# Performance work log

Hardware: AMD Instinct MI355X
Metric: run time of the kernel (lower is better)

## Reference

```python
import jax, jax.numpy as jnp
import numpy as np

N_SERIES = 1024  # N; x carries 3N stacked time-synchronous nodes
GCN_DEPTH = 2
IN_DIM = 64
H_DIM = 64


def setup_inputs() -> dict:
    key = jax.random.key(0)
    k = jax.random.split(key, 6)
    B, C, N3 = 64, IN_DIM, 3 * N_SERIES
    x = jax.random.normal(k[0], (N3, B, C), dtype=jnp.float32)
    A = jax.random.normal(k[1], (N3, N3), dtype=jnp.float32) * 0.02
    # Linear2d (1x1 conv) params per depth; act='glu' -> out = 2*h_dim
    s0 = 1.0 / np.sqrt(IN_DIM)
    s1 = 1.0 / np.sqrt(H_DIM)
    W0 = jax.random.uniform(k[2], (2 * H_DIM, IN_DIM), jnp.float32, -s0, s0)
    b0 = jax.random.uniform(k[3], (2 * H_DIM,), jnp.float32, -s0, s0)
    W1 = jax.random.uniform(k[4], (2 * H_DIM, H_DIM), jnp.float32, -s1, s1)
    b1 = jax.random.uniform(k[5], (2 * H_DIM,), jnp.float32, -s1, s1)
    return {"x": x, "A": A, "W0": W0, "b0": b0, "W1": W1, "b1": b1}


def reference(x, A, W0, b0, W1, b1):
    # x: (3N, B, C) -> (B, C, 3N)
    h = jnp.transpose(x, (1, 2, 0))
    convs = []
    for W, b in ((W0, b0), (W1, b1)):
        # GCN2d flow='tgt_to_src': h[b,c,v] = sum_w h[b,c,w] * A[v,w]  (L=1 squeezed)
        g = jnp.einsum('bcw,vw->bcv', h, A)
        # Linear2d 1x1 conv: channels C -> 2*h_dim, then GLU gate
        y = jnp.einsum('oc,bcv->bov', W, g) + b[None, :, None]
        lhs, rhs = jnp.split(y, 2, axis=1)
        h = lhs * jax.nn.sigmoid(rhs)          # (B, h_dim, 3N)
        convs.append(jnp.transpose(h, (2, 0, 1)))  # (3N, B, h_dim)
    # crop the middle N nodes of each depth, then max over depth
    cropped = jnp.stack([c[N_SERIES:2 * N_SERIES] for c in convs], axis=0)
    return jnp.max(cropped, axis=0)  # (N, B, h_dim)
```

## Files before the change

### kernel.cpp

```cpp
#include <hip/hip_runtime.h>
#include <hip/hip_bf16.h>
#include <stdint.h>

typedef __attribute__((ext_vector_type(8))) short s16x8;
typedef __attribute__((ext_vector_type(4))) float f32x4;
typedef __attribute__((ext_vector_type(8))) unsigned short u16x8;
typedef __attribute__((ext_vector_type(4))) unsigned short u16x4;

__device__ __forceinline__ float bf2f(unsigned short u) {
  union { uint32_t u; float f; } v; v.u = ((uint32_t)u) << 16; return v.f;
}
__device__ __forceinline__ unsigned short f2bf(float f) {
  union { float f; uint32_t u; } v; v.f = f;
  uint32_t u = v.u;
  return (unsigned short)((u + 0x7fffu + ((u >> 16) & 1u)) >> 16);
}
__device__ __forceinline__ void load_lds16(const void* g, void* l) {
  __builtin_amdgcn_global_load_lds(
      (const __attribute__((address_space(1))) void*)g,
      (__attribute__((address_space(3))) void*)l, 16, 0, 0);
}

template <int N>
__device__ __forceinline__ void vmw() {
  if constexpr (N == 0) asm volatile("s_waitcnt vmcnt(0)" ::: "memory");
  else if constexpr (N == 1) asm volatile("s_waitcnt vmcnt(1)" ::: "memory");
  else if constexpr (N == 2) asm volatile("s_waitcnt vmcnt(2)" ::: "memory");
  else if constexpr (N == 3) asm volatile("s_waitcnt vmcnt(3)" ::: "memory");
  else if constexpr (N == 4) asm volatile("s_waitcnt vmcnt(4)" ::: "memory");
  else if constexpr (N == 5) asm volatile("s_waitcnt vmcnt(5)" ::: "memory");
  else if constexpr (N == 6) asm volatile("s_waitcnt vmcnt(6)" ::: "memory");
  else if constexpr (N == 7) asm volatile("s_waitcnt vmcnt(7)" ::: "memory");
  else asm volatile("s_waitcnt vmcnt(8)" ::: "memory");
}
#define SBAR() asm volatile("s_barrier" ::: "memory")


__global__ void k_detect(const uint32_t* __restrict__ xw, int* __restrict__ flag) {
  int lane = threadIdx.x;
  uint32_t u = xw[lane * 97 + 1];
  int e = (u >> 7) & 0xFF;
  unsigned long long m = __ballot(e > 150);
  if (lane == 0) *flag = (__popcll(m) > 6) ? 1 : 0;
}

__global__ __launch_bounds__(256) void k_prep(const void* __restrict__ xin,
                                              const void* __restrict__ Ain,
                                              const void* __restrict__ W0,
                                              const void* __restrict__ b0,
                                              const void* __restrict__ W1,
                                              const void* __restrict__ b1,
                                              unsigned short* __restrict__ xtp,
                                              unsigned short* __restrict__ Abp,
                                              unsigned short* __restrict__ wb,
                                              const int* __restrict__ flag) {
  __shared__ __align__(16) unsigned short sh[64 * 65];
  const int t = threadIdx.x;
  const int bid = blockIdx.x;
  const int fp = *flag;

  if (bid < 3072) {
    const int w0 = (bid % 48) * 64;
    const int m0 = (bid / 48) * 64;
    if (fp) {
      const float* xf = (const float*)xin;
#pragma unroll
      for (int rep = 0; rep < 4; ++rep) {
        int vi = t + rep * 256;
        int r = vi >> 4;
        int c4 = (vi & 15) * 4;
        f32x4 v = *(const f32x4*)(xf + (uint64_t)(w0 + r) * 4096 + m0 + c4);
#pragma unroll
        for (int u = 0; u < 4; ++u) sh[(c4 + u) * 65 + r] = f2bf(v[u]);
      }
    } else {
      const unsigned short* xb = (const unsigned short*)xin;
#pragma unroll
      for (int rep = 0; rep < 2; ++rep) {
        int vi = t + rep * 256;
        int r = vi >> 3;
        int c8 = (vi & 7) * 8;
        u16x8 v = *(const u16x8*)(xb + (uint64_t)(w0 + r) * 4096 + m0 + c8);
#pragma unroll
        for (int u = 0; u < 8; ++u) sh[(c8 + u) * 65 + r] = v[u];
      }
    }
    __syncthreads();
    unsigned short* dst = xtp + ((uint64_t)(m0 >> 6) * 48 + (w0 >> 6)) * 4096;
#pragma unroll
    for (int rep = 0; rep < 2; ++rep) {
      int vi = t + rep * 256;
      int kb = vi >> 6, r = vi & 63;
      u16x8 v;
#pragma unroll
      for (int u = 0; u < 8; ++u) v[u] = sh[r * 65 + kb * 8 + u];
      *(u16x8*)(dst + kb * 512 + r * 8) = v;
    }
  } else if (bid < 5376) {
    const int b2 = bid - 3072;
    const int kt = b2 % 48, rt = b2 / 48;
    if (fp) {
      const float* Af = (const float*)Ain;
#pragma unroll
      for (int rep = 0; rep < 4; ++rep) {
        int vi = t + rep * 256;
        int r = vi >> 4;
        int c4 = (vi & 15) * 4;
        f32x4 v = *(const f32x4*)(Af + (uint64_t)(rt * 64 + r) * 3072 + kt * 64 + c4);
        int kb = c4 >> 3, e = c4 & 7;
#pragma unroll
        for (int u = 0; u < 4; ++u) sh[kb * 520 + r * 8 + e + u] = f2bf(v[u]);
      }
    } else {
      const unsigned short* Ab16 = (const unsigned short*)Ain;
#pragma unroll
      for (int rep = 0; rep < 2; ++rep) {
        int vi = t + rep * 256;
        int r = vi >> 3;
        int c8 = (vi & 7) * 8;
        u16x8 v = *(const u16x8*)(Ab16 + (uint64_t)(rt * 64 + r) * 3072 + kt * 64 + c8);
#pragma unroll
        for (int u = 0; u < 8; ++u) sh[(c8 >> 3) * 520 + r * 8 + u] = v[u];
      }
    }
    __syncthreads();
    unsigned short* dst = Abp + ((uint64_t)rt * 48 + kt) * 4096;
#pragma unroll
    for (int rep = 0; rep < 2; ++rep) {
      int vi = t + rep * 256;
      int kb = vi >> 6, r = vi & 63;
      u16x8 v;
#pragma unroll
      for (int u = 0; u < 8; ++u) v[u] = sh[kb * 520 + r * 8 + u];
      *(u16x8*)(dst + kb * 512 + r * 8) = v;
    }
  } else {
    for (int i = t; i < 16640; i += 256) {
      const void* src; int off;
      if (i < 8192)        { src = W0; off = i; }
      else if (i < 8320)   { src = b0; off = i - 8192; }
      else if (i < 16512)  { src = W1; off = i - 8320; }
      else                 { src = b1; off = i - 16512; }
      wb[i] = fp ? f2bf(((const float*)src)[off]) : ((const unsigned short*)src)[off];
    }
  }
}

template <int BM, int KTOT>
__global__ __launch_bounds__(512, 2) void k_gemm_glu2(
    const unsigned short* __restrict__ Am,
    const unsigned short* __restrict__ Bm,
    const unsigned short* __restrict__ W,
    const unsigned short* __restrict__ bias,
    unsigned short* __restrict__ H,
    int Vtot) {
  constexpr int BN  = 256;
  constexpr int IF  = BM / 32;
  constexpr int NPH = (IF > 4) ? 2 : 1;
  constexpr int IPH = IF / NPH;
  constexpr int APL = (BM / 64) * 4;
  constexpr int P   = APL + 16;
  constexpr int QF  = P / 8;
  constexpr int QR  = P - QF * 8;
  constexpr int PPW = QF + (QR ? 1 : 0);
  constexpr int BUFS = P * 512;
  constexpr int NT  = KTOT / 32;
  constexpr int Kt  = KTOT / 64;
  constexpr int NRB = BM / 16;
  constexpr int EPL = BM * 264;
  constexpr int SME = (4 * BUFS > EPL) ? 4 * BUFS : EPL;

  __shared__ __align__(16) unsigned short smem[SME];

  const int t    = threadIdx.x;
  const int lane = t & 63;
  const int wid  = t >> 6;
  const int wV   = wid >> 2;
  const int wM   = wid & 3;
  const int fr   = lane & 15;
  const int q4   = lane >> 4;
  const int v0   = blockIdx.x * BM;
  const int m0   = blockIdx.y * BN;
  const int art0 = v0 >> 6;
  const int brt0 = m0 >> 6;

  const int myq = QF + ((QR && wid < QR) ? 1 : 0);
  const unsigned short* srcb[PPW];
  int ldso[PPW];
#pragma unroll
  for (int q = 0; q < PPW; ++q) {
    int pi = wid + 8 * q;
    if (pi >= P) pi = P - 1;
    const int isA = pi < APL;
    const int rtl = (isA ? pi : pi - APL) >> 2;
    const int pb  = pi & 3;
    const unsigned short* base =
        isA ? (Am + (uint64_t)(art0 + rtl) * Kt * 4096)
            : (Bm + (uint64_t)(brt0 + rtl) * Kt * 4096);
    srcb[q] = base + pb * 512 + lane * 8;
    ldso[q] = pi * 512;
  }

  int aoff[IF], boff[4];
#pragma unroll
  for (int i = 0; i < IF; ++i) {
    const int row = wV * (BM / 2) + i * 16 + fr;
    aoff[i] = ((row >> 6) * 4 + q4) * 512 + (row & 63) * 8;
  }
#pragma unroll
  for (int j = 0; j < 4; ++j)
    boff[j] = (APL + wM * 4 + q4) * 512 + (j * 16 + fr) * 8;

  f32x4 acc[IF][4] = {};

#pragma unroll
  for (int pt = 0; pt < 3; ++pt)
#pragma unroll
    for (int q = 0; q < PPW; ++q)
      if (q < myq)
        load_lds16(srcb[q] + pt * 2048, smem + pt * BUFS + ldso[q]);
  if (QR && wid < QR) { vmw<2 * (QF + 1)>(); } else { vmw<2 * QF>(); }
  SBAR();

#pragma unroll 4
  for (int tt = 0; tt < NT; ++tt) {
    const unsigned short* buf = smem + (tt & 3) * BUFS;
    s16x8 bfr[4];
#pragma unroll
    for (int ph = 0; ph < NPH; ++ph) {
      if (ph == 0) {
#pragma unroll
        for (int j = 0; j < 4; ++j)
          bfr[j] = *(const s16x8*)(buf + boff[j]);
      }
      s16x8 afr[IPH];
#pragma unroll
      for (int ii = 0; ii < IPH; ++ii)
        afr[ii] = *(const s16x8*)(buf + aoff[ph * IPH + ii]);
      if (tt + 3 < NT) {
        unsigned short* dst = smem + ((tt + 3) & 3) * BUFS;
#pragma unroll
        for (int q = 0; q < PPW; ++q)
          if ((q % NPH) == ph && q < myq)
            load_lds16(srcb[q] + (uint64_t)(tt + 3) * 2048, dst + ldso[q]);
      }
      SBAR();
      __builtin_amdgcn_s_setprio(1);
#pragma unroll
      for (int ii = 0; ii < IPH; ++ii)
#pragma unroll
        for (int j = 0; j < 4; ++j)
          acc[ph * IPH + ii][j] = __builtin_amdgcn_mfma_f32_16x16x32_bf16(
              afr[ii], bfr[j], acc[ph * IPH + ii][j], 0, 0, 0);
      __builtin_amdgcn_s_setprio(0);
      if (ph == NPH - 1) {
        if (tt + 3 < NT) {
          if (QR && wid < QR) { vmw<2 * (QF + 1)>(); } else { vmw<2 * QF>(); }
        } else if (tt + 2 < NT) {
          if (QR && wid < QR) { vmw<QF + 1>(); } else { vmw<QF>(); }
        } else {
          vmw<0>();
        }
      }
      SBAR();
    }
  }

  {
    const int rr = q4 * 4;
#pragma unroll
    for (int i = 0; i < IF; ++i)
#pragma unroll
      for (int j = 0; j < 4; ++j) {
        const int col = wM * 64 + j * 16 + fr;
#pragma unroll
        for (int r = 0; r < 4; ++r) {
          const int row = wV * (BM / 2) + i * 16 + rr + r;
          smem[row * 264 + col] = f2bf(acc[i][j][r]);
        }
      }
  }
  __syncthreads();

  s16x8 wf[2][8];
#pragma unroll
  for (int ksi = 0; ksi < 2; ++ksi)
#pragma unroll
    for (int j = 0; j < 8; ++j)
      wf[ksi][j] = *(const s16x8*)(W + (j * 16 + fr) * 64 + ksi * 32 + q4 * 8);
  float bj[8];
#pragma unroll
  for (int j = 0; j < 8; ++j) bj[j] = bf2f(bias[j * 16 + fr]);

  const int Vt = Vtot >> 6;
#pragma unroll
  for (int rep = 0; rep < (NRB + 7) / 8; ++rep) {
    const int rb = rep * 8 + wid;
    if (rb < NRB) {
#pragma unroll
      for (int bb = 0; bb < 4; ++bb) {
        f32x4 acc2[8] = {};
#pragma unroll
        for (int ksi = 0; ksi < 2; ++ksi) {
          s16x8 af = *(const s16x8*)(smem + (rb * 16 + fr) * 264 + bb * 64 +
                                     ksi * 32 + q4 * 8);
#pragma unroll
          for (int j = 0; j < 8; ++j)
            acc2[j] = __builtin_amdgcn_mfma_f32_16x16x32_bf16(af, wf[ksi][j],
                                                              acc2[j], 0, 0, 0);
        }
        const int v = v0 + rb * 16 + q4 * 4;
#pragma unroll
        for (int j = 0; j < 4; ++j) {
          u16x4 pk;
#pragma unroll
          for (int r = 0; r < 4; ++r) {
            float lhs = acc2[j][r] + bj[j];
            float rhs = acc2[j + 4][r] + bj[j + 4];
            float sg = 1.0f / (1.0f + __expf(-rhs));
            pk[r] = f2bf(lhs * sg);
          }
          const int o = j * 16 + fr;
          const int hrow = m0 + bb * 64 + o;
          *(u16x4*)(H + ((uint64_t)(hrow >> 6) * Vt + (v >> 6)) * 4096 +
                    ((v >> 3) & 7) * 512 + (hrow & 63) * 8 + (v & 7)) = pk;
        }
      }
    }
  }
}

__global__ __launch_bounds__(256) void k_maxout(const unsigned short* __restrict__ H1,
                                                const unsigned short* __restrict__ H2,
                                                float* __restrict__ out) {
  __shared__ __align__(16) float tile[64 * 65];
  const int t = threadIdx.x;
  const int b = blockIdx.y;
  const int n0 = blockIdx.x * 64;
  {
    int j = t >> 2, p = t & 3;
    int c1 = 1024 + n0 + p * 16;
    int c2 = n0 + p * 16;
    const unsigned short* h1p =
        H1 + ((uint64_t)b * 48 + (c1 >> 6)) * 4096 + ((c1 >> 3) & 7) * 512 + j * 8;
    const unsigned short* h2p =
        H2 + ((uint64_t)b * 16 + (c2 >> 6)) * 4096 + ((c2 >> 3) & 7) * 512 + j * 8;
    u16x8 a0 = *(const u16x8*)(h1p);
    u16x8 a1 = *(const u16x8*)(h1p + 512);
    u16x8 c0 = *(const u16x8*)(h2p);
    u16x8 c1v = *(const u16x8*)(h2p + 512);
#pragma unroll
    for (int u = 0; u < 8; ++u) {
      tile[j * 65 + p * 16 + u] = fmaxf(bf2f(a0[u]), bf2f(c0[u]));
      tile[j * 65 + p * 16 + 8 + u] = fmaxf(bf2f(a1[u]), bf2f(c1v[u]));
    }
  }
  __syncthreads();
  {
    int n = t >> 2, jb = (t & 3) * 16;
    float* op = out + (uint64_t)(n0 + n) * 4096 + b * 64 + jb;
#pragma unroll
    for (int q = 0; q < 4; ++q) {
      f32x4 o;
#pragma unroll
      for (int u = 0; u < 4; ++u) o[u] = tile[(jb + q * 4 + u) * 65 + n];
      *(f32x4*)(op + q * 4) = o;
    }
  }
}

extern "C" void kernel_launch(void* const* d_in, const int* in_sizes, int n_in,
                              void* d_out, int out_size, void* d_ws, size_t ws_size,
                              hipStream_t stream) {
  (void)in_sizes; (void)n_in; (void)out_size; (void)ws_size;
  const void* x  = d_in[0];
  const void* A  = d_in[1];
  const void* W0 = d_in[2];
  const void* b0 = d_in[3];
  const void* W1 = d_in[4];
  const void* b1 = d_in[5];
  float* out = (float*)d_out;

  char* ws = (char*)d_ws;
  unsigned short* Xtp = (unsigned short*)(ws + 0);
  unsigned short* H2p = (unsigned short*)(ws + 0);
  unsigned short* Abp = (unsigned short*)(ws + 25165824);
  unsigned short* Wb  = (unsigned short*)(ws + 44040192);
  unsigned short* H1p = (unsigned short*)(ws + 44105728);
  int* flag = (int*)(ws + 69271552);

  k_detect<<<1, 64, 0, stream>>>((const uint32_t*)x, flag);
  k_prep<<<5377, 256, 0, stream>>>(x, A, W0, b0, W1, b1, Xtp, Abp, Wb, flag);
  k_gemm_glu2<192, 3072><<<dim3(16, 16), 512, 0, stream>>>(
      Abp, Xtp, Wb, Wb + 8192, H1p, 3072);
  k_gemm_glu2<64, 3072><<<dim3(16, 16), 512, 0, stream>>>(
      Abp + (uint64_t)16 * 48 * 4096, H1p, Wb + 8320, Wb + 16512, H2p, 1024);
  k_maxout<<<dim3(16, 64), 256, 0, stream>>>(H1p, H2p, out);
}
```

Before: 274.8 us.

## Software-pipeline LDS fragment loads in GEMM and fold dtype detection into prep

Measured after the change: 280.1 us. Within noise of the previous version (+2.0%).

```diff
diff --git a/kernel.cpp b/kernel.cpp
--- a/kernel.cpp
+++ b/kernel.cpp
@@ -36,14 +36,6 @@
 #define SBAR() asm volatile("s_barrier" ::: "memory")
 
 
-__global__ void k_detect(const uint32_t* __restrict__ xw, int* __restrict__ flag) {
-  int lane = threadIdx.x;
-  uint32_t u = xw[lane * 97 + 1];
-  int e = (u >> 7) & 0xFF;
-  unsigned long long m = __ballot(e > 150);
-  if (lane == 0) *flag = (__popcll(m) > 6) ? 1 : 0;
-}
-
 __global__ __launch_bounds__(256) void k_prep(const void* __restrict__ xin,
                                               const void* __restrict__ Ain,
                                               const void* __restrict__ W0,
@@ -52,12 +44,17 @@
                                               const void* __restrict__ b1,
                                               unsigned short* __restrict__ xtp,
                                               unsigned short* __restrict__ Abp,
-                                              unsigned short* __restrict__ wb,
-                                              const int* __restrict__ flag) {
+                                              unsigned short* __restrict__ wb) {
   __shared__ __align__(16) unsigned short sh[64 * 65];
   const int t = threadIdx.x;
   const int bid = blockIdx.x;
-  const int fp = *flag;
+  int fp;
+  {
+    uint32_t u = ((const uint32_t*)xin)[(t & 63) * 97 + 1];
+    int e = (u >> 7) & 0xFF;
+    unsigned long long m = __ballot(e > 150);
+    fp = (__popcll(m) > 6) ? 1 : 0;
+  }
 
   if (bid < 3072) {
     const int w0 = (bid % 48) * 64;
@@ -147,7 +144,7 @@
 }
 
 template <int BM, int KTOT>
-__global__ __launch_bounds__(512, 2) void k_gemm_glu2(
+__global__ __launch_bounds__(512, 2) void k_gemm_glu3(
     const unsigned short* __restrict__ Am,
     const unsigned short* __restrict__ Bm,
     const unsigned short* __restrict__ W,
@@ -222,50 +219,128 @@
   if (QR && wid < QR) { vmw<2 * (QF + 1)>(); } else { vmw<2 * QF>(); }
   SBAR();
 
-#pragma unroll 4
-  for (int tt = 0; tt < NT; ++tt) {
-    const unsigned short* buf = smem + (tt & 3) * BUFS;
-    s16x8 bfr[4];
-#pragma unroll
-    for (int ph = 0; ph < NPH; ++ph) {
-      if (ph == 0) {
+  s16x8 bcur[4], a0[IPH];
+#pragma unroll
+  for (int j = 0; j < 4; ++j) bcur[j] = *(const s16x8*)(smem + boff[j]);
+#pragma unroll
+  for (int i = 0; i < IPH; ++i) a0[i] = *(const s16x8*)(smem + aoff[i]);
+  s16x8 a1[IPH];
+
+#pragma unroll 2
+  for (int tt = 0; tt < NT - 1; ++tt) {
+    const unsigned short* buf  = smem + (tt & 3) * BUFS;
+    const unsigned short* bufn = smem + ((tt + 1) & 3) * BUFS;
+    unsigned short* pdst = smem + ((tt + 3) & 3) * BUFS;
+    if constexpr (NPH == 2) {
+#pragma unroll
+      for (int i = 0; i < IPH; ++i)
+        a1[i] = *(const s16x8*)(buf + aoff[IPH + i]);
+      if (tt + 3 < NT) {
+#pragma unroll
+        for (int q = 0; q < PPW; ++q)
+          if ((q & 1) == 0 && q < myq)
+            load_lds16(srcb[q] + (uint64_t)(tt + 3) * 2048, pdst + ldso[q]);
+      }
+      SBAR();
+      __builtin_amdgcn_s_setprio(1);
+#pragma unroll
+      for (int i = 0; i < IPH; ++i)
 #pragma unroll
         for (int j = 0; j < 4; ++j)
-          bfr[j] = *(const s16x8*)(buf + boff[j]);
-      }
-      s16x8 afr[IPH];
-#pragma unroll
-      for (int ii = 0; ii < IPH; ++ii)
-        afr[ii] = *(const s16x8*)(buf + aoff[ph * IPH + ii]);
+          acc[i][j] = __builtin_amdgcn_mfma_f32_16x16x32_bf16(a0[i], bcur[j],
+                                                              acc[i][j], 0, 0, 0);
+      __builtin_amdgcn_s_setprio(0);
+      SBAR();
       if (tt + 3 < NT) {
-        unsigned short* dst = smem + ((tt + 3) & 3) * BUFS;
 #pragma unroll
         for (int q = 0; q < PPW; ++q)
-          if ((q % NPH) == ph && q < myq)
-            load_lds16(srcb[q] + (uint64_t)(tt + 3) * 2048, dst + ldso[q]);
-      }
-      SBAR();
+          if ((q & 1) == 1 && q < myq)
+            load_lds16(srcb[q] + (uint64_t)(tt + 3) * 2048, pdst + ldso[q]);
+        if (QR && wid < QR) { vmw<2 * (QF + 1)>(); } else { vmw<2 * QF>(); }
+      } else if (tt + 2 < NT) {
+        if (QR && wid < QR) { vmw<QF + 1>(); } else { vmw<QF>(); }
+      } else {
+        vmw<0>();
+      }
+      SBAR();
+      s16x8 bnxt[4], a0n[IPH];
+#pragma unroll
+      for (int j = 0; j < 4; ++j) bnxt[j] = *(const s16x8*)(bufn + boff[j]);
+#pragma unroll
+      for (int i = 0; i < IPH; ++i) a0n[i] = *(const s16x8*)(bufn + aoff[i]);
       __builtin_amdgcn_s_setprio(1);
 #pragma unroll
-      for (int ii = 0; ii < IPH; ++ii)
+      for (int i = 0; i < IPH; ++i)
 #pragma unroll
         for (int j = 0; j < 4; ++j)
-          acc[ph * IPH + ii][j] = __builtin_amdgcn_mfma_f32_16x16x32_bf16(
-              afr[ii], bfr[j], acc[ph * IPH + ii][j], 0, 0, 0);
+          acc[IPH + i][j] = __builtin_amdgcn_mfma_f32_16x16x32_bf16(
+              a1[i], bcur[j], acc[IPH + i][j], 0, 0, 0);
       __builtin_amdgcn_s_setprio(0);
-      if (ph == NPH - 1) {
-        if (tt + 3 < NT) {
-          if (QR && wid < QR) { vmw<2 * (QF + 1)>(); } else { vmw<2 * QF>(); }
-        } else if (tt + 2 < NT) {
-          if (QR && wid < QR) { vmw<QF + 1>(); } else { vmw<QF>(); }
-        } else {
-          vmw<0>();
-        }
-      }
-      SBAR();
-    }
-  }
-
+      SBAR();
+#pragma unroll
+      for (int j = 0; j < 4; ++j) bcur[j] = bnxt[j];
+#pragma unroll
+      for (int i = 0; i < IPH; ++i) a0[i] = a0n[i];
+    } else {
+      if (tt + 3 < NT) {
+#pragma unroll
+        for (int q = 0; q < PPW; ++q)
+          if (q < myq)
+            load_lds16(srcb[q] + (uint64_t)(tt + 3) * 2048, pdst + ldso[q]);
+        if (QR && wid < QR) { vmw<2 * (QF + 1)>(); } else { vmw<2 * QF>(); }
+      } else if (tt + 2 < NT) {
+        if (QR && wid < QR) { vmw<QF + 1>(); } else { vmw<QF>(); }
+      } else {
+        vmw<0>();
+      }
+      SBAR();
+      s16x8 bnxt[4], a0n[IPH];
+#pragma unroll
+      for (int j = 0; j < 4; ++j) bnxt[j] = *(const s16x8*)(bufn + boff[j]);
+#pragma unroll
+      for (int i = 0; i < IPH; ++i) a0n[i] = *(const s16x8*)(bufn + aoff[i]);
+      __builtin_amdgcn_s_setprio(1);
+#pragma unroll
+      for (int i = 0; i < IPH; ++i)
+#pragma unroll
+        for (int j = 0; j < 4; ++j)
+          acc[i][j] = __builtin_amdgcn_mfma_f32_16x16x32_bf16(a0[i], bcur[j],
+                                                              acc[i][j], 0, 0, 0);
+      __builtin_amdgcn_s_setprio(0);
+      SBAR();
+#pragma unroll
+      for (int j = 0; j < 4; ++j) bcur[j] = bnxt[j];
+#pragma unroll
+      for (int i = 0; i < IPH; ++i) a0[i] = a0n[i];
+    }
+  }
+  if constexpr (NPH == 2) {
+    const unsigned short* buf = smem + ((NT - 1) & 3) * BUFS;
+#pragma unroll
+    for (int i = 0; i < IPH; ++i)
+      a1[i] = *(const s16x8*)(buf + aoff[IPH + i]);
+#pragma unroll
+    for (int i = 0; i < IPH; ++i)
+#pragma unroll
+      for (int j = 0; j < 4; ++j)
+        acc[i][j] = __builtin_amdgcn_mfma_f32_16x16x32_bf16(a0[i], bcur[j],
+                                                            acc[i][j], 0, 0, 0);
+#pragma unroll
+    for (int i = 0; i < IPH; ++i)
+#pragma unroll
+      for (int j = 0; j < 4; ++j)
+        acc[IPH + i][j] = __builtin_amdgcn_mfma_f32_16x16x32_bf16(
+            a1[i], bcur[j], acc[IPH + i][j], 0, 0, 0);
+  } else {
+#pragma unroll
+    for (int i = 0; i < IPH; ++i)
+#pragma unroll
+      for (int j = 0; j < 4; ++j)
+        acc[i][j] = __builtin_amdgcn_mfma_f32_16x16x32_bf16(a0[i], bcur[j],
+                                                            acc[i][j], 0, 0, 0);
+  }
+
+  __syncthreads();
   {
     const int rr = q4 * 4;
 #pragma unroll
@@ -388,12 +463,12 @@
   unsigned short* Wb  = (unsigned short*)(ws + 44040192);
   unsigned short* H1p = (unsigned short*)(ws + 44105728);
   int* flag = (int*)(ws + 69271552);
-
-  k_detect<<<1, 64, 0, stream>>>((const uint32_t*)x, flag);
-  k_prep<<<5377, 256, 0, stream>>>(x, A, W0, b0, W1, b1, Xtp, Abp, Wb, flag);
-  k_gemm_glu2<192, 3072><<<dim3(16, 16), 512, 0, stream>>>(
+  (void)flag;
+
+  k_prep<<<5377, 256, 0, stream>>>(x, A, W0, b0, W1, b1, Xtp, Abp, Wb);
+  k_gemm_glu3<192, 3072><<<dim3(16, 16), 512, 0, stream>>>(
       Abp, Xtp, Wb, Wb + 8192, H1p, 3072);
-  k_gemm_glu2<64, 3072><<<dim3(16, 16), 512, 0, stream>>>(
+  k_gemm_glu3<64, 3072><<<dim3(16, 16), 512, 0, stream>>>(
       Abp + (uint64_t)16 * 48 * 4096, H1p, Wb + 8320, Wb + 16512, H2p, 1024);
   k_maxout<<<dim3(16, 64), 256, 0, stream>>>(H1p, H2p, out);
 }
```

## Fuse max-over-depth into second GEMM epilogue and inline dtype detection

Applied to the files above, without the earlier changes.

New measurement: 261.5 us. 1.05x faster.

```diff
diff --git a/kernel.cpp b/kernel.cpp
--- a/kernel.cpp
+++ b/kernel.cpp
@@ -36,14 +36,6 @@
 #define SBAR() asm volatile("s_barrier" ::: "memory")
 
 
-__global__ void k_detect(const uint32_t* __restrict__ xw, int* __restrict__ flag) {
-  int lane = threadIdx.x;
-  uint32_t u = xw[lane * 97 + 1];
-  int e = (u >> 7) & 0xFF;
-  unsigned long long m = __ballot(e > 150);
-  if (lane == 0) *flag = (__popcll(m) > 6) ? 1 : 0;
-}
-
 __global__ __launch_bounds__(256) void k_prep(const void* __restrict__ xin,
                                               const void* __restrict__ Ain,
                                               const void* __restrict__ W0,
@@ -52,12 +44,17 @@
                                               const void* __restrict__ b1,
                                               unsigned short* __restrict__ xtp,
                                               unsigned short* __restrict__ Abp,
-                                              unsigned short* __restrict__ wb,
-                                              const int* __restrict__ flag) {
+                                              unsigned short* __restrict__ wb) {
   __shared__ __align__(16) unsigned short sh[64 * 65];
   const int t = threadIdx.x;
   const int bid = blockIdx.x;
-  const int fp = *flag;
+  int fp;
+  {
+    uint32_t u = ((const uint32_t*)xin)[(t & 63) * 97 + 1];
+    int e = (u >> 7) & 0xFF;
+    unsigned long long m = __ballot(e > 150);
+    fp = (__popcll(m) > 6) ? 1 : 0;
+  }
 
   if (bid < 3072) {
     const int w0 = (bid % 48) * 64;
@@ -146,18 +143,18 @@
   }
 }
 
-template <int BM, int KTOT>
-__global__ __launch_bounds__(512, 2) void k_gemm_glu2(
+template <int BM, int KTOT, bool FUSEMAX>
+__global__ __launch_bounds__(512, 2) void k_gemm_glu4(
     const unsigned short* __restrict__ Am,
     const unsigned short* __restrict__ Bm,
     const unsigned short* __restrict__ W,
     const unsigned short* __restrict__ bias,
     unsigned short* __restrict__ H,
+    const unsigned short* __restrict__ Hprev,
+    float* __restrict__ outp,
     int Vtot) {
   constexpr int BN  = 256;
   constexpr int IF  = BM / 32;
-  constexpr int NPH = (IF > 4) ? 2 : 1;
-  constexpr int IPH = IF / NPH;
   constexpr int APL = (BM / 64) * 4;
   constexpr int P   = APL + 16;
   constexpr int QF  = P / 8;
@@ -225,47 +222,37 @@
 #pragma unroll 4
   for (int tt = 0; tt < NT; ++tt) {
     const unsigned short* buf = smem + (tt & 3) * BUFS;
-    s16x8 bfr[4];
-#pragma unroll
-    for (int ph = 0; ph < NPH; ++ph) {
-      if (ph == 0) {
-#pragma unroll
-        for (int j = 0; j < 4; ++j)
-          bfr[j] = *(const s16x8*)(buf + boff[j]);
-      }
-      s16x8 afr[IPH];
-#pragma unroll
-      for (int ii = 0; ii < IPH; ++ii)
-        afr[ii] = *(const s16x8*)(buf + aoff[ph * IPH + ii]);
-      if (tt + 3 < NT) {
-        unsigned short* dst = smem + ((tt + 3) & 3) * BUFS;
-#pragma unroll
-        for (int q = 0; q < PPW; ++q)
-          if ((q % NPH) == ph && q < myq)
-            load_lds16(srcb[q] + (uint64_t)(tt + 3) * 2048, dst + ldso[q]);
-      }
-      SBAR();
-      __builtin_amdgcn_s_setprio(1);
-#pragma unroll
-      for (int ii = 0; ii < IPH; ++ii)
-#pragma unroll
-        for (int j = 0; j < 4; ++j)
-          acc[ph * IPH + ii][j] = __builtin_amdgcn_mfma_f32_16x16x32_bf16(
-              afr[ii], bfr[j], acc[ph * IPH + ii][j], 0, 0, 0);
-      __builtin_amdgcn_s_setprio(0);
-      if (ph == NPH - 1) {
-        if (tt + 3 < NT) {
-          if (QR && wid < QR) { vmw<2 * (QF + 1)>(); } else { vmw<2 * QF>(); }
-        } else if (tt + 2 < NT) {
-          if (QR && wid < QR) { vmw<QF + 1>(); } else { vmw<QF>(); }
-        } else {
-          vmw<0>();
-        }
-      }
-      SBAR();
-    }
-  }
-
+    s16x8 bfr[4], afr[IF];
+#pragma unroll
+    for (int j = 0; j < 4; ++j) bfr[j] = *(const s16x8*)(buf + boff[j]);
+#pragma unroll
+    for (int i = 0; i < IF; ++i) afr[i] = *(const s16x8*)(buf + aoff[i]);
+    if (tt + 3 < NT) {
+      unsigned short* pdst = smem + ((tt + 3) & 3) * BUFS;
+#pragma unroll
+      for (int q = 0; q < PPW; ++q)
+        if (q < myq)
+          load_lds16(srcb[q] + (uint64_t)(tt + 3) * 2048, pdst + ldso[q]);
+    }
+    __builtin_amdgcn_s_setprio(1);
+#pragma unroll
+    for (int i = 0; i < IF; ++i)
+#pragma unroll
+      for (int j = 0; j < 4; ++j)
+        acc[i][j] = __builtin_amdgcn_mfma_f32_16x16x32_bf16(afr[i], bfr[j],
+                                                            acc[i][j], 0, 0, 0);
+    __builtin_amdgcn_s_setprio(0);
+    if (tt + 3 < NT) {
+      if (QR && wid < QR) { vmw<2 * (QF + 1)>(); } else { vmw<2 * QF>(); }
+    } else if (tt + 2 < NT) {
+      if (QR && wid < QR) { vmw<QF + 1>(); } else { vmw<QF>(); }
+    } else {
+      vmw<0>();
+    }
+    SBAR();
+  }
+
+  __syncthreads();
   {
     const int rr = q4 * 4;
 #pragma unroll
@@ -312,59 +299,35 @@
         const int v = v0 + rb * 16 + q4 * 4;
 #pragma unroll
         for (int j = 0; j < 4; ++j) {
-          u16x4 pk;
-#pragma unroll
-          for (int r = 0; r < 4; ++r) {
-            float lhs = acc2[j][r] + bj[j];
-            float rhs = acc2[j + 4][r] + bj[j + 4];
-            float sg = 1.0f / (1.0f + __expf(-rhs));
-            pk[r] = f2bf(lhs * sg);
-          }
           const int o = j * 16 + fr;
           const int hrow = m0 + bb * 64 + o;
-          *(u16x4*)(H + ((uint64_t)(hrow >> 6) * Vt + (v >> 6)) * 4096 +
-                    ((v >> 3) & 7) * 512 + (hrow & 63) * 8 + (v & 7)) = pk;
+          if constexpr (FUSEMAX) {
+            const int c = 1024 + v;
+            u16x4 hv = *(const u16x4*)(Hprev +
+                ((uint64_t)(hrow >> 6) * 48 + (c >> 6)) * 4096 +
+                ((c >> 3) & 7) * 512 + (hrow & 63) * 8 + (c & 7));
+            float* op = outp + (uint64_t)v * 4096 + hrow;
+#pragma unroll
+            for (int r = 0; r < 4; ++r) {
+              float lhs = acc2[j][r] + bj[j];
+              float rhs = acc2[j + 4][r] + bj[j + 4];
+              float sg = 1.0f / (1.0f + __expf(-rhs));
+              op[(uint64_t)r * 4096] = fmaxf(lhs * sg, bf2f(hv[r]));
+            }
+          } else {
+            u16x4 pk;
+#pragma unroll
+            for (int r = 0; r < 4; ++r) {
+              float lhs = acc2[j][r] + bj[j];
+              float rhs = acc2[j + 4][r] + bj[j + 4];
+              float sg = 1.0f / (1.0f + __expf(-rhs));
+              pk[r] = f2bf(lhs * sg);
+            }
+            *(u16x4*)(H + ((uint64_t)(hrow >> 6) * Vt + (v >> 6)) * 4096 +
+                      ((v >> 3) & 7) * 512 + (hrow & 63) * 8 + (v & 7)) = pk;
+          }
         }
       }
-    }
-  }
-}
-
-__global__ __launch_bounds__(256) void k_maxout(const unsigned short* __restrict__ H1,
-                                                const unsigned short* __restrict__ H2,
-                                                float* __restrict__ out) {
-  __shared__ __align__(16) float tile[64 * 65];
-  const int t = threadIdx.x;
-  const int b = blockIdx.y;
-  const int n0 = blockIdx.x * 64;
-  {
-    int j = t >> 2, p = t & 3;
-    int c1 = 1024 + n0 + p * 16;
-    int c2 = n0 + p * 16;
-    const unsigned short* h1p =
-        H1 + ((uint64_t)b * 48 + (c1 >> 6)) * 4096 + ((c1 >> 3) & 7) * 512 + j * 8;
-    const unsigned short* h2p =
-        H2 + ((uint64_t)b * 16 + (c2 >> 6)) * 4096 + ((c2 >> 3) & 7) * 512 + j * 8;
-    u16x8 a0 = *(const u16x8*)(h1p);
-    u16x8 a1 = *(const u16x8*)(h1p + 512);
-    u16x8 c0 = *(const u16x8*)(h2p);
-    u16x8 c1v = *(const u16x8*)(h2p + 512);
-#pragma unroll
-    for (int u = 0; u < 8; ++u) {
-      tile[j * 65 + p * 16 + u] = fmaxf(bf2f(a0[u]), bf2f(c0[u]));
-      tile[j * 65 + p * 16 + 8 + u] = fmaxf(bf2f(a1[u]), bf2f(c1v[u]));
-    }
-  }
-  __syncthreads();
-  {
-    int n = t >> 2, jb = (t & 3) * 16;
-    float* op = out + (uint64_t)(n0 + n) * 4096 + b * 64 + jb;
-#pragma unroll
-    for (int q = 0; q < 4; ++q) {
-      f32x4 o;
-#pragma unroll
-      for (int u = 0; u < 4; ++u) o[u] = tile[(jb + q * 4 + u) * 65 + n];
-      *(f32x4*)(op + q * 4) = o;
     }
   }
 }
@@ -383,17 +346,14 @@
 
   char* ws = (char*)d_ws;
   unsigned short* Xtp = (unsigned short*)(ws + 0);
-  unsigned short* H2p = (unsigned short*)(ws + 0);
   unsigned short* Abp = (unsigned short*)(ws + 25165824);
   unsigned short* Wb  = (unsigned short*)(ws + 44040192);
   unsigned short* H1p = (unsigned short*)(ws + 44105728);
-  int* flag = (int*)(ws + 69271552);
-
-  k_detect<<<1, 64, 0, stream>>>((const uint32_t*)x, flag);
-  k_prep<<<5377, 256, 0, stream>>>(x, A, W0, b0, W1, b1, Xtp, Abp, Wb, flag);
-  k_gemm_glu2<192, 3072><<<dim3(16, 16), 512, 0, stream>>>(
-      Abp, Xtp, Wb, Wb + 8192, H1p, 3072);
-  k_gemm_glu2<64, 3072><<<dim3(16, 16), 512, 0, stream>>>(
-      Abp + (uint64_t)16 * 48 * 4096, H1p, Wb + 8320, Wb + 16512, H2p, 1024);
-  k_maxout<<<dim3(16, 64), 256, 0, stream>>>(H1p, H2p, out);
-}
+
+  k_prep<<<5377, 256, 0, stream>>>(x, A, W0, b0, W1, b1, Xtp, Abp, Wb);
+  k_gemm_glu4<192, 3072, false><<<dim3(16, 16), 512, 0, stream>>>(
+      Abp, Xtp, Wb, Wb + 8192, H1p, nullptr, nullptr, 3072);
+  k_gemm_glu4<64, 3072, true><<<dim3(16, 16), 512, 0, stream>>>(
+      Abp + (uint64_t)16 * 48 * 4096, H1p, Wb + 8320, Wb + 16512,
+      nullptr, H1p, out, 1024);
+}
```
